# Kernel tuning notes

Hardware: AMD Instinct MI355X
Metric: run time of the kernel (lower is better)

The kernel has to match this reference:

```python
import jax, jax.numpy as jnp
import numpy as np
import math

D_MODEL = 1024
N_HEADS = 16
D_K = D_MODEL // N_HEADS
NB_FEATURES = max(1, math.ceil(math.log(D_MODEL)))  # 7
D_FF = 4096
BH = 4  # block_size_h
BW = 4  # block_size_w
EPS_LN = 1e-6


def gelu_approx(x):
    c = math.sqrt(2.0 / math.pi)
    return 0.5 * x * (1.0 + jnp.tanh(c * (x + 0.044715 * x * x * x)))


def layer_norm(x, alpha, bias):
    # torch .std() uses ddof=1 (unbiased)
    mean = x.mean(axis=-1, keepdims=True)
    std = jnp.std(x, axis=-1, ddof=1, keepdims=True)
    return alpha * (x - mean) / (std + EPS_LN) + bias


def causal_performer(q_in, k_in, v_in, wq, wk, wv, wo, omega):
    B, Sq, D = q_in.shape
    Sk = k_in.shape[1]
    q = (q_in @ wq.T).reshape(B, Sq, N_HEADS, D_K)
    k = (k_in @ wk.T).reshape(B, Sk, N_HEADS, D_K)
    v = (v_in @ wv.T).reshape(B, Sk, N_HEADS, D_K)
    # exp kernel feature map: exp(-0.5 * (x @ omega^T)^2)
    qp = jnp.exp(-0.5 * jnp.square(q @ omega.T))  # (B,Sq,H,nb)
    kp = jnp.exp(-0.5 * jnp.square(k @ omega.T))  # (B,Sk,H,nb)
    qp = qp / (qp.sum(-1, keepdims=True) + 1e-6)
    kp = kp / (kp.sum(-1, keepdims=True) + 1e-6)
    K_cum = jnp.cumsum(kp, axis=1)                               # (B,Sk,H,nb)
    KV_cum = jnp.cumsum(kp[..., None] * v[..., None, :], axis=1)  # (B,Sk,H,nb,dk)
    key_idx = jnp.clip((jnp.arange(Sq) // BH + 1) * BW - 1, None, Sk - 1)
    K_sel = K_cum[:, key_idx]    # (B,Sq,H,nb)
    KV_sel = KV_cum[:, key_idx]  # (B,Sq,H,nb,dk)
    num = jnp.einsum('bshn,bshnd->bshd', qp, KV_sel)
    den = jnp.einsum('bshn,bshn->bsh', qp, K_sel)[..., None]
    out = (num / (den + 1e-6)).reshape(B, Sq, D)
    return out @ wo.T


def setup_inputs() -> dict:
    key = jax.random.key(0)
    ks = jax.random.split(key, 24)
    s = 0.02
    p = {}
    p['x'] = jax.random.normal(ks[0], (2, 4096, D_MODEL), jnp.float32)
    p['lto'] = jax.random.normal(ks[1], (2, 4096, D_MODEL), jnp.float32)
    for i, nm in enumerate(['wq_s', 'wk_s', 'wv_s', 'wo_s']):
        p[nm] = jax.random.normal(ks[2 + i], (D_MODEL, D_MODEL), jnp.float32) * s
    for i, nm in enumerate(['wq_c', 'wk_c', 'wv_c', 'wo_c']):
        p[nm] = jax.random.normal(ks[6 + i], (D_MODEL, D_MODEL), jnp.float32) * s
    p['omega_s'] = jax.random.normal(ks[10], (NB_FEATURES, D_K), jnp.float32) / math.sqrt(D_K)
    p['omega_c'] = jax.random.normal(ks[11], (NB_FEATURES, D_K), jnp.float32) / math.sqrt(D_K)
    p['w1'] = jax.random.normal(ks[12], (D_FF, D_MODEL), jnp.float32) * s
    p['b1'] = jnp.zeros((D_FF,), jnp.float32)
    p['w2'] = jax.random.normal(ks[13], (D_MODEL, D_FF), jnp.float32) * s
    p['b2'] = jnp.zeros((D_MODEL,), jnp.float32)
    for i in range(3):
        p[f'ln{i}_a'] = jnp.ones((D_MODEL,), jnp.float32)
        p[f'ln{i}_b'] = jnp.zeros((D_MODEL,), jnp.float32)
    return p


def reference(x, lto, wq_s, wk_s, wv_s, wo_s, wq_c, wk_c, wv_c, wo_c,
              omega_s, omega_c, w1, b1, w2, b2,
              ln0_a, ln0_b, ln1_a, ln1_b, ln2_a, ln2_b):
    # residual 0: self-attention on x
    xn = layer_norm(x, ln0_a, ln0_b)
    x = x + causal_performer(xn, xn, xn, wq_s, wk_s, wv_s, wo_s, omega_s)
    # residual 1: cross-attention, queries = normed lto, keys/values = updated x
    ln = layer_norm(lto, ln1_a, ln1_b)
    lto = lto + causal_performer(ln, x, x, wq_c, wk_c, wv_c, wo_c, omega_c)
    # residual 2: feed-forward
    fn = layer_norm(lto, ln2_a, ln2_b)
    ff = gelu_approx(fn @ w1.T + b1) @ w2.T + b2
    return lto + ff
```

## Files before the change

### kernel.cpp

```cpp
#include <hip/hip_runtime.h>
#include <cstdint>
#include <cstddef>

typedef __bf16 bf16;
typedef __bf16 bf16x8 __attribute__((ext_vector_type(8)));
typedef __bf16 bf16x4 __attribute__((ext_vector_type(4)));
typedef float  f32x4  __attribute__((ext_vector_type(4)));

#define NB 7
static constexpr int Bq = 2, Sq = 4096, Dm = 1024, Dff = 4096;
static constexpr int Mrows = Bq * Sq;
static constexpr int NCH = Sq / 4;
static constexpr int CSW = 464;

template <int V> struct ic { static constexpr int value = V; };

__device__ __forceinline__ void gload16(const void* g, void* l) {
  __builtin_amdgcn_global_load_lds((__attribute__((address_space(1))) void*)g,
                                   (__attribute__((address_space(3))) void*)l,
                                   16, 0, 0);
}

template <int N> __device__ __forceinline__ void wait_vmcnt() {
  asm volatile("s_waitcnt vmcnt(%0)" :: "n"(N) : "memory");
}
__device__ __forceinline__ void wait_lgkm0() {
  asm volatile("s_waitcnt lgkmcnt(0)" ::: "memory");
}
__device__ __forceinline__ void SB() { __builtin_amdgcn_sched_barrier(0); }

__device__ __forceinline__ float gelu_f(float x) {
  const float c = 0.79788456080286535588f;
  float z = c * (x + 0.044715f * x * x * x);
  float t = 1.f - 2.f / (__expf(2.f * z) + 1.f);
  return 0.5f * x * (1.f + t);
}

struct CvtA {
  const float* s[10];
  bf16* d[10];
  int start[11];
};
__global__ __launch_bounds__(256) void cvt10(CvtA a) {
  const int i = blockIdx.x * 256 + threadIdx.x;
  int r = 0;
#pragma unroll
  for (int k = 1; k < 10; ++k) r += (i >= a.start[k]);
  const int o = i - a.start[r];
  f32x4 v = *(const f32x4*)&a.s[r][(size_t)o * 4];
  bf16x4 ov;
#pragma unroll
  for (int e = 0; e < 4; ++e) ov[e] = (bf16)v[e];
  *(bf16x4*)&a.d[r][(size_t)o * 4] = ov;
}

__global__ __launch_bounds__(256) void ln_kernel(const float* __restrict__ x,
                                                 const float* __restrict__ alpha,
                                                 const float* __restrict__ beta,
                                                 bf16* __restrict__ out) {
  const int row = blockIdx.x, tid = threadIdx.x;
  const float* xr = x + (size_t)row * Dm;
  f32x4 v = *(const f32x4*)&xr[tid * 4];
  float s  = v[0] + v[1] + v[2] + v[3];
  float s2 = v[0]*v[0] + v[1]*v[1] + v[2]*v[2] + v[3]*v[3];
#pragma unroll
  for (int o = 32; o > 0; o >>= 1) { s += __shfl_xor(s, o); s2 += __shfl_xor(s2, o); }
  __shared__ float red[8];
  const int wid = tid >> 6, lane = tid & 63;
  if (lane == 0) { red[wid] = s; red[wid + 4] = s2; }
  __syncthreads();
  s  = red[0] + red[1] + red[2] + red[3];
  s2 = red[4] + red[5] + red[6] + red[7];
  const float mean = s * (1.f / 1024.f);
  float var = (s2 - s * mean) * (1.f / 1023.f);
  var = fmaxf(var, 0.f);
  const float inv = 1.f / (sqrtf(var) + 1e-6f);
  f32x4 a4 = *(const f32x4*)&alpha[tid * 4];
  f32x4 b4 = *(const f32x4*)&beta[tid * 4];
  bf16x4 o4;
#pragma unroll
  for (int e = 0; e < 4; ++e) o4[e] = (bf16)(a4[e] * (v[e] - mean) * inv + b4[e]);
  *(bf16x4*)&out[(size_t)row * Dm + tid * 4] = o4;
}

template <int MODE>
__global__ __launch_bounds__(256, 2) void gemm128(
    const bf16* __restrict__ A, const bf16* __restrict__ Bw,
    int M, int N, int K,
    const float* __restrict__ bias, const float* __restrict__ res,
    float* __restrict__ outF, bf16* __restrict__ outB) {
  __shared__ __align__(16) char lds[65536];

  const int tid = threadIdx.x;
  const int lane = tid & 63, wid = tid >> 6;
  const int wm = wid >> 1, wn = wid & 1;

  const int nwg = gridDim.x;
  const int nc = N >> 7;
  const int nsc = nc >> 3;
  const int lin = (blockIdx.x & 7) * (nwg >> 3) + (blockIdx.x >> 3);
  const int s = lin >> 6, w = lin & 63;
  const int sr = s / nsc, sc = s - sr * nsc;
  const int bm = (sr * 8 + (w >> 3)) * 128;
  const int bn = (sc * 8 + (w & 7)) * 128;
  const int NT = K >> 6;

  const int srow = tid >> 3;
  const int scol = ((tid & 7) ^ (srow & 7)) * 8;
  const bf16* pSA = A  + (size_t)(bm + srow) * K + scol;
  const bf16* pSB = Bw + (size_t)(bn + srow) * K + scol;
  const size_t cK = (size_t)32 * K;
  const int stDa = wid * 1024;

  auto stage = [&](int buf, const bf16* sa, const bf16* sb) {
#pragma unroll
    for (int c = 0; c < 4; ++c) {
      gload16(sa + (size_t)c * cK, &lds[buf * 16384 + c * 4096 + stDa]);
      gload16(sb + (size_t)c * cK, &lds[32768 + buf * 16384 + c * 4096 + stDa]);
    }
  };

  const int lr = lane & 15, uo = lane >> 4;
  const int rdA0 = (wm * 64 + lr) * 128 + ((uo)     ^ (lr & 7)) * 16;
  const int rdA1 = (wm * 64 + lr) * 128 + ((4 + uo) ^ (lr & 7)) * 16;
  const int rdB0 = 32768 + (wn * 64 + lr) * 128 + ((uo)     ^ (lr & 7)) * 16;
  const int rdB1 = 32768 + (wn * 64 + lr) * 128 + ((4 + uo) ^ (lr & 7)) * 16;

  f32x4 acc[4][4] = {};
  bf16x8 a[4][2], b[4][2];

  stage(0, pSA, pSB);
  stage(1, pSA + 64, pSB + 64);
  pSA += 128; pSB += 128;
  wait_vmcnt<8>();
  __builtin_amdgcn_s_barrier();

  auto TILE = [&](auto BUFC, int tt) {
    constexpr int BUF = decltype(BUFC)::value;
#pragma unroll
    for (int i = 0; i < 4; ++i) {
      a[i][0] = *(const bf16x8*)&lds[rdA0 + BUF * 16384 + i * 2048];
      a[i][1] = *(const bf16x8*)&lds[rdA1 + BUF * 16384 + i * 2048];
    }
#pragma unroll
    for (int j = 0; j < 4; ++j) {
      b[j][0] = *(const bf16x8*)&lds[rdB0 + BUF * 16384 + j * 2048];
      b[j][1] = *(const bf16x8*)&lds[rdB1 + BUF * 16384 + j * 2048];
    }
    wait_lgkm0(); SB();
    __builtin_amdgcn_s_barrier(); SB();

    if (tt + 2 < NT) stage(BUF, pSA + (size_t)(tt & 1) * 64,
                                pSB + (size_t)(tt & 1) * 64);
#pragma unroll
    for (int i = 0; i < 4; ++i)
#pragma unroll
      for (int j = 0; j < 4; ++j) {
        acc[i][j] = __builtin_amdgcn_mfma_f32_16x16x32_bf16(a[i][0], b[j][0], acc[i][j], 0, 0, 0);
        acc[i][j] = __builtin_amdgcn_mfma_f32_16x16x32_bf16(a[i][1], b[j][1], acc[i][j], 0, 0, 0);
      }
    SB();
    if (tt < NT - 2) wait_vmcnt<8>();
    else             wait_vmcnt<0>();
    __builtin_amdgcn_s_barrier(); SB();
  };

  for (int t = 0; t < NT; t += 2) {
    TILE(ic<0>{}, t);
    TILE(ic<1>{}, t + 1);
    pSA += 128; pSB += 128;
  }

#pragma unroll
  for (int f = 0; f < 4; ++f) {
    const int r0 = bm + wm * 64 + f * 16 + (lane >> 4) * 4;
#pragma unroll
    for (int g = 0; g < 4; ++g) {
      const int c = bn + wn * 64 + g * 16 + (lane & 15);
      float bv = 0.f;
      if (MODE == 3 || MODE == 4) bv = bias[c];
#pragma unroll
      for (int r = 0; r < 4; ++r) {
        const size_t idx = (size_t)(r0 + r) * N + c;
        float v = acc[f][g][r];
        if (MODE == 1 || MODE == 2) v += res[idx];
        if (MODE == 3) v = gelu_f(v + bv);
        if (MODE == 4) v += bv + res[idx];
        if (MODE == 0 || MODE == 1 || MODE == 3) outB[idx] = (bf16)v;
        else outF[idx] = v;
      }
    }
  }
}

__global__ __launch_bounds__(512) void perf_cs(
    const bf16* __restrict__ kmat, const bf16* __restrict__ vmat, int ld,
    const float* __restrict__ omega, bf16* __restrict__ CS,
    float* __restrict__ segtot) {
  const int tid = threadIdx.x;
  const int bh = blockIdx.y, b = bh >> 4, h = bh & 15;
  const int seg = blockIdx.x;
  const int s0 = seg * 512;
  __shared__ __align__(16) bf16 vs[512][64];
  __shared__ float kps[512][8];
  __shared__ float oms[448];

  {
    const bf16* vb = vmat + ((size_t)(b * Sq + s0)) * ld + h * 64;
#pragma unroll
    for (int p = 0; p < 8; ++p) {
      const int row = p * 64 + (tid >> 3), c16 = (tid & 7) * 8;
      *(uint4*)&vs[row][c16 ^ ((row & 7) * 8)] =
          *(const uint4*)&vb[(size_t)row * ld + c16];
    }
  }
  if (tid < 448) oms[tid] = omega[tid];
  __syncthreads();

  {
    const int row = tid;
    const bf16* kr = kmat + ((size_t)(b * Sq + s0 + row)) * ld + h * 64;
    bf16x8 kv[8];
#pragma unroll
    for (int q = 0; q < 8; ++q) kv[q] = *(const bf16x8*)&kr[q * 8];
    float f[NB];
#pragma unroll
    for (int n = 0; n < NB; ++n) f[n] = 0.f;
#pragma unroll
    for (int d = 0; d < 64; ++d) {
      const float kd = (float)kv[d >> 3][d & 7];
#pragma unroll
      for (int n = 0; n < NB; ++n) f[n] += kd * oms[n * 64 + d];
    }
    float sum = 1e-6f, e[NB];
#pragma unroll
    for (int n = 0; n < NB; ++n) { e[n] = __expf(-0.5f * f[n] * f[n]); sum += e[n]; }
    const float inv = 1.f / sum;
#pragma unroll
    for (int n = 0; n < NB; ++n) kps[row][n] = e[n] * inv;
    kps[row][7] = 0.f;
  }
  __syncthreads();

  if (tid < CSW) {
    const int comp = tid;
    bf16* outb = CS + ((size_t)bh * NCH + seg * 128) * CSW;
    float r = 0.f;
    if (comp < 8) {
      for (int c = 0; c < 128; ++c) {
        if (comp < 7)
          r += kps[4*c][comp] + kps[4*c+1][comp] + kps[4*c+2][comp] + kps[4*c+3][comp];
        outb[(size_t)c * CSW + comp] = (bf16)r;
      }
    } else if (comp < 456) {
      const int n = (comp - 8) >> 6, d = (comp - 8) & 63;
      for (int c = 0; c < 128; ++c) {
#pragma unroll
        for (int i = 0; i < 4; ++i) {
          const int row = 4 * c + i;
          r += kps[row][n] * (float)vs[row][d ^ ((row & 7) * 8)];
        }
        outb[(size_t)c * CSW + comp] = (bf16)r;
      }
    } else {
      for (int c = 0; c < 128; ++c) outb[(size_t)c * CSW + comp] = (bf16)0.f;
    }
    segtot[((size_t)bh * 8 + seg) * CSW + comp] = r;
  }
}

__global__ __launch_bounds__(256) void perf_out(
    const bf16* __restrict__ qmat, int ldq, const float* __restrict__ omega,
    const bf16* __restrict__ CS, const float* __restrict__ segtot,
    bf16* __restrict__ attn) {
  const int tid = threadIdx.x;
  const int bh = blockIdx.y, b = bh >> 4, h = bh & 15;
  const int s0 = blockIdx.x * 128;
  const int cg0 = s0 >> 2;
  const int seg = cg0 >> 7;
  __shared__ __align__(16) float Ps[32 * CSW];
  __shared__ float qps[128][8];
  __shared__ float oms[NB * 64];
  __shared__ float offs[CSW];

  for (int c = tid; c < CSW; c += 256) {
    float o = 0.f;
    for (int ss = 0; ss < seg; ++ss) o += segtot[((size_t)bh * 8 + ss) * CSW + c];
    offs[c] = o;
  }
  if (tid < 224) { oms[tid] = omega[tid]; oms[tid + 224] = omega[tid + 224]; }
  __syncthreads();

  {
    const bf16* src = CS + ((size_t)bh * NCH + cg0) * CSW;
    for (int i = tid; i < 32 * CSW / 4; i += 256) {
      bf16x4 a4 = *(const bf16x4*)&src[(size_t)i * 4];
      const int c0 = (i % (CSW / 4)) * 4;
      f32x4 o;
#pragma unroll
      for (int e = 0; e < 4; ++e) o[e] = (float)a4[e] + offs[c0 + e];
      *(f32x4*)&Ps[i * 4] = o;
    }
  }
  __syncthreads();
  {
    const int p = tid >> 1, half = tid & 1;
    const bf16* qr = qmat + ((size_t)(b * Sq + s0 + p)) * ldq + h * 64 + half * 32;
    bf16x8 qv[4];
#pragma unroll
    for (int q = 0; q < 4; ++q) qv[q] = *(const bf16x8*)&qr[q * 8];
    float f[NB];
#pragma unroll
    for (int n = 0; n < NB; ++n) f[n] = 0.f;
#pragma unroll
    for (int d = 0; d < 32; ++d) {
      float qd = (float)qv[d >> 3][d & 7];
#pragma unroll
      for (int n = 0; n < NB; ++n) f[n] += qd * oms[n * 64 + half * 32 + d];
    }
    float sum = 1e-6f;
    float e[NB];
#pragma unroll
    for (int n = 0; n < NB; ++n) {
      float full = f[n] + __shfl_xor(f[n], 1);
      e[n] = __expf(-0.5f * full * full);
      sum += e[n];
    }
    float inv = 1.f / sum;
    if (half == 0) {
      float den = 1e-6f;
      const float* Pr = &Ps[(p >> 2) * CSW];
#pragma unroll
      for (int n = 0; n < NB; ++n) {
        float qn = e[n] * inv;
        qps[p][n] = qn;
        den += qn * Pr[n];
      }
      qps[p][7] = 1.f / den;
    }
  }
  __syncthreads();
  {
    const int d = tid & 63, w = tid >> 6;
    for (int qq = w; qq < 128; qq += 4) {
      const float* Pr = &Ps[(qq >> 2) * CSW + 8 + d];
      float num = 0.f;
#pragma unroll
      for (int n = 0; n < NB; ++n) num += qps[qq][n] * Pr[n * 64];
      attn[((size_t)(b * Sq + s0 + qq)) * Dm + h * 64 + d] = (bf16)(num * qps[qq][7]);
    }
  }
}

extern "C" void kernel_launch(void* const* d_in, const int* in_sizes, int n_in,
                              void* d_out, int out_size, void* d_ws, size_t ws_size,
                              hipStream_t stream) {
  const float* x    = (const float*)d_in[0];
  const float* lto  = (const float*)d_in[1];
  const float* w_s[4] = {(const float*)d_in[2], (const float*)d_in[3],
                         (const float*)d_in[4], (const float*)d_in[5]};
  const float* w_c[4] = {(const float*)d_in[6], (const float*)d_in[7],
                         (const float*)d_in[8], (const float*)d_in[9]};
  const float* omega_s = (const float*)d_in[10];
  const float* omega_c = (const float*)d_in[11];
  const float* w1 = (const float*)d_in[12];
  const float* b1 = (const float*)d_in[13];
  const float* w2 = (const float*)d_in[14];
  const float* b2 = (const float*)d_in[15];
  const float* ln_a[3] = {(const float*)d_in[16], (const float*)d_in[18], (const float*)d_in[20]};
  const float* ln_b[3] = {(const float*)d_in[17], (const float*)d_in[19], (const float*)d_in[21]};

  char* ws = (char*)d_ws;
  size_t off = 0;
  auto alloc = [&](size_t bytes) -> char* {
    char* p = ws + off;
    off += (bytes + 255) & ~(size_t)255;
    return p;
  };

  const size_t actB = (size_t)Mrows * Dm * sizeof(bf16);
  const size_t MB32 = (size_t)Mrows * 2048 * sizeof(bf16);

  bf16* wqkv = (bf16*)alloc((size_t)3072 * 1024 * 2);
  bf16* wo_sb = (bf16*)alloc((size_t)1024 * 1024 * 2);
  bf16* wq_cb = (bf16*)alloc((size_t)1024 * 1024 * 2);
  bf16* wkv  = (bf16*)alloc((size_t)2048 * 1024 * 2);
  bf16* wo_cb = (bf16*)alloc((size_t)1024 * 1024 * 2);
  bf16* w1b = (bf16*)alloc((size_t)Dff * Dm * 2);
  bf16* w2b = (bf16*)alloc((size_t)Dff * Dm * 2);
  bf16* xnb  = (bf16*)alloc(actB);
  char* pool = alloc((size_t)Mrows * Dff * 2);
  bf16* qkvb = (bf16*)pool;
  bf16* kvb  = (bf16*)pool;
  bf16* qb   = (bf16*)(pool + MB32);
  bf16* hb   = (bf16*)pool;
  bf16* attnb= (bf16*)alloc(actB);
  bf16* x2b  = (bf16*)alloc(actB);
  bf16* ln1b = (bf16*)alloc(actB);
  float* lto2 = (float*)alloc((size_t)Mrows * Dm * 4);
  bf16*  CSb  = (bf16*)alloc((size_t)32 * NCH * CSW * 2);
  float* stb  = (float*)alloc((size_t)32 * 8 * CSW * 4);
  bf16* fnb = xnb;

  {
    CvtA a;
    const float* srcs[10] = {w_s[0], w_s[1], w_s[2], w_s[3], w_c[0],
                             w_c[1], w_c[2], w_c[3], w1, w2};
    bf16* dsts[10] = {wqkv, wqkv + 1048576, wqkv + 2097152, wo_sb, wq_cb,
                      wkv, wkv + 1048576, wo_cb, w1b, w2b};
    const int SM = 262144, LG = 1048576;
    int st = 0;
    for (int i = 0; i < 10; ++i) {
      a.s[i] = srcs[i]; a.d[i] = dsts[i]; a.start[i] = st;
      st += (i < 8) ? SM : LG;
    }
    a.start[10] = st;
    cvt10<<<st / 256, 256, 0, stream>>>(a);
  }

  dim3 gperf(Sq / 128, Bq * 16);
  dim3 gseg(8, Bq * 16);
  const int gQKV = (Mrows / 128) * (3072 / 128);
  const int gKV  = (Mrows / 128) * (2048 / 128);
  const int gFF1 = (Mrows / 128) * (4096 / 128);
  const int gN1k = (Mrows / 128) * (1024 / 128);

  ln_kernel<<<Mrows, 256, 0, stream>>>(x, ln_a[0], ln_b[0], xnb);
  gemm128<0><<<gQKV, 256, 0, stream>>>(xnb, wqkv, Mrows, 3072, 1024, nullptr, nullptr, nullptr, qkvb);
  perf_cs<<<gseg, 512, 0, stream>>>(qkvb + 1024, qkvb + 2048, 3072, omega_s, CSb, stb);
  perf_out<<<gperf, 256, 0, stream>>>(qkvb, 3072, omega_s, CSb, stb, attnb);
  gemm128<1><<<gN1k, 256, 0, stream>>>(attnb, wo_sb, Mrows, 1024, 1024, nullptr, x, nullptr, x2b);

  ln_kernel<<<Mrows, 256, 0, stream>>>(lto, ln_a[1], ln_b[1], ln1b);
  gemm128<0><<<gN1k, 256, 0, stream>>>(ln1b, wq_cb, Mrows, 1024, 1024, nullptr, nullptr, nullptr, qb);
  gemm128<0><<<gKV, 256, 0, stream>>>(x2b, wkv, Mrows, 2048, 1024, nullptr, nullptr, nullptr, kvb);
  perf_cs<<<gseg, 512, 0, stream>>>(kvb, kvb + 1024, 2048, omega_c, CSb, stb);
  perf_out<<<gperf, 256, 0, stream>>>(qb, 1024, omega_c, CSb, stb, attnb);
  gemm128<2><<<gN1k, 256, 0, stream>>>(attnb, wo_cb, Mrows, 1024, 1024, nullptr, lto, lto2, nullptr);

  ln_kernel<<<Mrows, 256, 0, stream>>>(lto2, ln_a[2], ln_b[2], fnb);
  gemm128<3><<<gFF1, 256, 0, stream>>>(fnb, w1b, Mrows, 4096, 1024, b1, nullptr, nullptr, hb);
  gemm128<4><<<gN1k, 256, 0, stream>>>(hb, w2b, Mrows, 1024, 4096, b2, lto2, (float*)d_out, nullptr);
}
```

Measured before the change: 500.0 us.

## Add 256x256-tile GEMM kernel for wide QKV, KV and FF1 projections

Adds a 512-thread GEMM with 256x256 output tiles, 128 KB of double-buffered LDS and an 8x4 MFMA fragment per wave. It is used for the QKV, KV and FF1 GEMMs, with the GELU-plus-bias epilogue moved there from the 128-tile kernel. Larger tiles raise arithmetic intensity per LDS and global load and cut the number of workgroups. In exchange, only one block fits per CU, register pressure rises, and the QKV grid of 384 tiles leaves a partial second wave.

Measured after the change: 529.0 us. 5.8% more time.

```diff
diff --git a/kernel.cpp b/kernel.cpp
--- a/kernel.cpp
+++ b/kernel.cpp
@@ -84,6 +84,112 @@
 }
 
 template <int MODE>
+__global__ __launch_bounds__(512, 2) void gemm256(
+    const bf16* __restrict__ A, const bf16* __restrict__ Bw,
+    int M, int N, int K,
+    const float* __restrict__ bias, bf16* __restrict__ outB) {
+  __shared__ __align__(16) char lds[131072];
+
+  const int tid = threadIdx.x;
+  const int lane = tid & 63, wid = tid >> 6;
+  const int wm = wid >> 2, wn = wid & 3;
+
+  const int nwg = gridDim.x;
+  const int nc = N >> 8;
+  const int nsc = nc >> 2;
+  const int lin = (blockIdx.x & 7) * (nwg >> 3) + (blockIdx.x >> 3);
+  const int s = lin >> 4, w = lin & 15;
+  const int sr = s / nsc, sc = s - sr * nsc;
+  const int bm = (sr * 4 + (w >> 2)) * 256;
+  const int bn = (sc * 4 + (w & 3)) * 256;
+  const int NT = K >> 6;
+
+  const int srow = tid >> 3;
+  const int scol = ((tid & 7) ^ (srow & 7)) * 8;
+  const bf16* pSA = A  + (size_t)(bm + srow) * K + scol;
+  const bf16* pSB = Bw + (size_t)(bn + srow) * K + scol;
+  const size_t cK = (size_t)64 * K;
+  const int stDa = wid * 1024;
+
+  auto stage = [&](int buf, const bf16* sa, const bf16* sb) {
+#pragma unroll
+    for (int c = 0; c < 4; ++c) {
+      gload16(sa + (size_t)c * cK, &lds[buf * 32768 + c * 8192 + stDa]);
+      gload16(sb + (size_t)c * cK, &lds[65536 + buf * 32768 + c * 8192 + stDa]);
+    }
+  };
+
+  const int lr = lane & 15, uo = lane >> 4;
+  const int rA0 = (wm * 128 + lr) * 128 + ((uo)     ^ (lr & 7)) * 16;
+  const int rA1 = (wm * 128 + lr) * 128 + ((4 + uo) ^ (lr & 7)) * 16;
+  const int rB0 = 65536 + (wn * 64 + lr) * 128 + ((uo)     ^ (lr & 7)) * 16;
+  const int rB1 = 65536 + (wn * 64 + lr) * 128 + ((4 + uo) ^ (lr & 7)) * 16;
+
+  f32x4 acc[8][4] = {};
+  bf16x8 a[8][2], b[4][2];
+
+  stage(0, pSA, pSB);
+  stage(1, pSA + 64, pSB + 64);
+  pSA += 128; pSB += 128;
+  wait_vmcnt<8>();
+  __builtin_amdgcn_s_barrier();
+
+  auto TILE = [&](auto BUFC, int tt) {
+    constexpr int BUF = decltype(BUFC)::value;
+#pragma unroll
+    for (int i = 0; i < 8; ++i) {
+      a[i][0] = *(const bf16x8*)&lds[rA0 + BUF * 32768 + i * 2048];
+      a[i][1] = *(const bf16x8*)&lds[rA1 + BUF * 32768 + i * 2048];
+    }
+#pragma unroll
+    for (int j = 0; j < 4; ++j) {
+      b[j][0] = *(const bf16x8*)&lds[rB0 + BUF * 32768 + j * 2048];
+      b[j][1] = *(const bf16x8*)&lds[rB1 + BUF * 32768 + j * 2048];
+    }
+    wait_lgkm0(); SB();
+    __builtin_amdgcn_s_barrier(); SB();
+
+    if (tt + 2 < NT) stage(BUF, pSA + (size_t)(tt & 1) * 64,
+                                pSB + (size_t)(tt & 1) * 64);
+#pragma unroll
+    for (int i = 0; i < 8; ++i)
+#pragma unroll
+      for (int j = 0; j < 4; ++j) {
+        acc[i][j] = __builtin_amdgcn_mfma_f32_16x16x32_bf16(a[i][0], b[j][0], acc[i][j], 0, 0, 0);
+        acc[i][j] = __builtin_amdgcn_mfma_f32_16x16x32_bf16(a[i][1], b[j][1], acc[i][j], 0, 0, 0);
+      }
+    SB();
+    if (tt < NT - 2) wait_vmcnt<8>();
+    else             wait_vmcnt<0>();
+    __builtin_amdgcn_s_barrier(); SB();
+  };
+
+  for (int t = 0; t < NT; t += 2) {
+    TILE(ic<0>{}, t);
+    TILE(ic<1>{}, t + 1);
+    pSA += 128; pSB += 128;
+  }
+
+#pragma unroll
+  for (int f = 0; f < 8; ++f) {
+    const int r0 = bm + wm * 128 + f * 16 + (lane >> 4) * 4;
+#pragma unroll
+    for (int g = 0; g < 4; ++g) {
+      const int c = bn + wn * 64 + g * 16 + (lane & 15);
+      float bv = 0.f;
+      if (MODE == 3) bv = bias[c];
+#pragma unroll
+      for (int r = 0; r < 4; ++r) {
+        const size_t idx = (size_t)(r0 + r) * N + c;
+        float v = acc[f][g][r];
+        if (MODE == 3) v = gelu_f(v + bv);
+        outB[idx] = (bf16)v;
+      }
+    }
+  }
+}
+
+template <int MODE>
 __global__ __launch_bounds__(256, 2) void gemm128(
     const bf16* __restrict__ A, const bf16* __restrict__ Bw,
     int M, int N, int K,
@@ -178,15 +284,14 @@
     for (int g = 0; g < 4; ++g) {
       const int c = bn + wn * 64 + g * 16 + (lane & 15);
       float bv = 0.f;
-      if (MODE == 3 || MODE == 4) bv = bias[c];
+      if (MODE == 4) bv = bias[c];
 #pragma unroll
       for (int r = 0; r < 4; ++r) {
         const size_t idx = (size_t)(r0 + r) * N + c;
         float v = acc[f][g][r];
         if (MODE == 1 || MODE == 2) v += res[idx];
-        if (MODE == 3) v = gelu_f(v + bv);
         if (MODE == 4) v += bv + res[idx];
-        if (MODE == 0 || MODE == 1 || MODE == 3) outB[idx] = (bf16)v;
+        if (MODE == 0 || MODE == 1) outB[idx] = (bf16)v;
         else outF[idx] = v;
       }
     }
@@ -420,25 +525,25 @@
 
   dim3 gperf(Sq / 128, Bq * 16);
   dim3 gseg(8, Bq * 16);
-  const int gQKV = (Mrows / 128) * (3072 / 128);
-  const int gKV  = (Mrows / 128) * (2048 / 128);
-  const int gFF1 = (Mrows / 128) * (4096 / 128);
+  const int gQKV = (Mrows / 256) * (3072 / 256);
+  const int gKV  = (Mrows / 256) * (2048 / 256);
+  const int gFF1 = (Mrows / 256) * (4096 / 256);
   const int gN1k = (Mrows / 128) * (1024 / 128);
 
   ln_kernel<<<Mrows, 256, 0, stream>>>(x, ln_a[0], ln_b[0], xnb);
-  gemm128<0><<<gQKV, 256, 0, stream>>>(xnb, wqkv, Mrows, 3072, 1024, nullptr, nullptr, nullptr, qkvb);
+  gemm256<0><<<gQKV, 512, 0, stream>>>(xnb, wqkv, Mrows, 3072, 1024, nullptr, qkvb);
   perf_cs<<<gseg, 512, 0, stream>>>(qkvb + 1024, qkvb + 2048, 3072, omega_s, CSb, stb);
   perf_out<<<gperf, 256, 0, stream>>>(qkvb, 3072, omega_s, CSb, stb, attnb);
   gemm128<1><<<gN1k, 256, 0, stream>>>(attnb, wo_sb, Mrows, 1024, 1024, nullptr, x, nullptr, x2b);
 
   ln_kernel<<<Mrows, 256, 0, stream>>>(lto, ln_a[1], ln_b[1], ln1b);
   gemm128<0><<<gN1k, 256, 0, stream>>>(ln1b, wq_cb, Mrows, 1024, 1024, nullptr, nullptr, nullptr, qb);
-  gemm128<0><<<gKV, 256, 0, stream>>>(x2b, wkv, Mrows, 2048, 1024, nullptr, nullptr, nullptr, kvb);
+  gemm256<0><<<gKV, 512, 0, stream>>>(x2b, wkv, Mrows, 2048, 1024, nullptr, kvb);
   perf_cs<<<gseg, 512, 0, stream>>>(kvb, kvb + 1024, 2048, omega_c, CSb, stb);
   perf_out<<<gperf, 256, 0, stream>>>(qb, 1024, omega_c, CSb, stb, attnb);
   gemm128<2><<<gN1k, 256, 0, stream>>>(attnb, wo_cb, Mrows, 1024, 1024, nullptr, lto, lto2, nullptr);
 
   ln_kernel<<<Mrows, 256, 0, stream>>>(lto2, ln_a[2], ln_b[2], fnb);
-  gemm128<3><<<gFF1, 256, 0, stream>>>(fnb, w1b, Mrows, 4096, 1024, b1, nullptr, nullptr, hb);
+  gemm256<3><<<gFF1, 512, 0, stream>>>(fnb, w1b, Mrows, 4096, 1024, b1, hb);
   gemm128<4><<<gN1k, 256, 0, stream>>>(hb, w2b, Mrows, 1024, 4096, b2, lto2, (float*)d_out, nullptr);
 }
```

## Replace double-buffered GEMM pipeline with single-buffered loop and higher occupancy

Applied to the files above, without the earlier changes.

The bf16 GEMM drops its two-stage LDS double buffer, with its explicit vmcnt waits and sched barriers, and uses a simple loop. Each K-tile is loaded into a single 32 KB LDS buffer between two __syncthreads, then consumed by the MFMAs. Halving LDS and raising launch_bounds to 3 blocks per CU is meant to rely on more resident workgroups to hide memory latency. The cost is that each workgroup no longer overlaps its own global loads with compute, and it now takes two full barriers per tile.

Measured after the change: 532.7 us. 6.5% more time.

```diff
diff --git a/kernel.cpp b/kernel.cpp
--- a/kernel.cpp
+++ b/kernel.cpp
@@ -13,21 +13,11 @@
 static constexpr int NCH = Sq / 4;
 static constexpr int CSW = 464;
 
-template <int V> struct ic { static constexpr int value = V; };
-
 __device__ __forceinline__ void gload16(const void* g, void* l) {
   __builtin_amdgcn_global_load_lds((__attribute__((address_space(1))) void*)g,
                                    (__attribute__((address_space(3))) void*)l,
                                    16, 0, 0);
 }
-
-template <int N> __device__ __forceinline__ void wait_vmcnt() {
-  asm volatile("s_waitcnt vmcnt(%0)" :: "n"(N) : "memory");
-}
-__device__ __forceinline__ void wait_lgkm0() {
-  asm volatile("s_waitcnt lgkmcnt(0)" ::: "memory");
-}
-__device__ __forceinline__ void SB() { __builtin_amdgcn_sched_barrier(0); }
 
 __device__ __forceinline__ float gelu_f(float x) {
   const float c = 0.79788456080286535588f;
@@ -84,12 +74,12 @@
 }
 
 template <int MODE>
-__global__ __launch_bounds__(256, 2) void gemm128(
+__global__ __launch_bounds__(256, 3) void gemm128(
     const bf16* __restrict__ A, const bf16* __restrict__ Bw,
     int M, int N, int K,
     const float* __restrict__ bias, const float* __restrict__ res,
     float* __restrict__ outF, bf16* __restrict__ outB) {
-  __shared__ __align__(16) char lds[65536];
+  __shared__ __align__(16) char lds[32768];
 
   const int tid = threadIdx.x;
   const int lane = tid & 63, wid = tid >> 6;
@@ -112,46 +102,34 @@
   const size_t cK = (size_t)32 * K;
   const int stDa = wid * 1024;
 
-  auto stage = [&](int buf, const bf16* sa, const bf16* sb) {
-#pragma unroll
-    for (int c = 0; c < 4; ++c) {
-      gload16(sa + (size_t)c * cK, &lds[buf * 16384 + c * 4096 + stDa]);
-      gload16(sb + (size_t)c * cK, &lds[32768 + buf * 16384 + c * 4096 + stDa]);
-    }
-  };
-
   const int lr = lane & 15, uo = lane >> 4;
   const int rdA0 = (wm * 64 + lr) * 128 + ((uo)     ^ (lr & 7)) * 16;
   const int rdA1 = (wm * 64 + lr) * 128 + ((4 + uo) ^ (lr & 7)) * 16;
-  const int rdB0 = 32768 + (wn * 64 + lr) * 128 + ((uo)     ^ (lr & 7)) * 16;
-  const int rdB1 = 32768 + (wn * 64 + lr) * 128 + ((4 + uo) ^ (lr & 7)) * 16;
+  const int rdB0 = 16384 + (wn * 64 + lr) * 128 + ((uo)     ^ (lr & 7)) * 16;
+  const int rdB1 = 16384 + (wn * 64 + lr) * 128 + ((4 + uo) ^ (lr & 7)) * 16;
 
   f32x4 acc[4][4] = {};
-  bf16x8 a[4][2], b[4][2];
-
-  stage(0, pSA, pSB);
-  stage(1, pSA + 64, pSB + 64);
-  pSA += 128; pSB += 128;
-  wait_vmcnt<8>();
-  __builtin_amdgcn_s_barrier();
-
-  auto TILE = [&](auto BUFC, int tt) {
-    constexpr int BUF = decltype(BUFC)::value;
+
+  for (int t = 0; t < NT; ++t) {
+    __syncthreads();
+#pragma unroll
+    for (int c = 0; c < 4; ++c) {
+      gload16(pSA + (size_t)c * cK, &lds[c * 4096 + stDa]);
+      gload16(pSB + (size_t)c * cK, &lds[16384 + c * 4096 + stDa]);
+    }
+    __syncthreads();
+
+    bf16x8 a[4][2], b[4][2];
 #pragma unroll
     for (int i = 0; i < 4; ++i) {
-      a[i][0] = *(const bf16x8*)&lds[rdA0 + BUF * 16384 + i * 2048];
-      a[i][1] = *(const bf16x8*)&lds[rdA1 + BUF * 16384 + i * 2048];
+      a[i][0] = *(const bf16x8*)&lds[rdA0 + i * 2048];
+      a[i][1] = *(const bf16x8*)&lds[rdA1 + i * 2048];
     }
 #pragma unroll
     for (int j = 0; j < 4; ++j) {
-      b[j][0] = *(const bf16x8*)&lds[rdB0 + BUF * 16384 + j * 2048];
-      b[j][1] = *(const bf16x8*)&lds[rdB1 + BUF * 16384 + j * 2048];
-    }
-    wait_lgkm0(); SB();
-    __builtin_amdgcn_s_barrier(); SB();
-
-    if (tt + 2 < NT) stage(BUF, pSA + (size_t)(tt & 1) * 64,
-                                pSB + (size_t)(tt & 1) * 64);
+      b[j][0] = *(const bf16x8*)&lds[rdB0 + j * 2048];
+      b[j][1] = *(const bf16x8*)&lds[rdB1 + j * 2048];
+    }
 #pragma unroll
     for (int i = 0; i < 4; ++i)
 #pragma unroll
@@ -159,16 +137,7 @@
         acc[i][j] = __builtin_amdgcn_mfma_f32_16x16x32_bf16(a[i][0], b[j][0], acc[i][j], 0, 0, 0);
         acc[i][j] = __builtin_amdgcn_mfma_f32_16x16x32_bf16(a[i][1], b[j][1], acc[i][j], 0, 0, 0);
       }
-    SB();
-    if (tt < NT - 2) wait_vmcnt<8>();
-    else             wait_vmcnt<0>();
-    __builtin_amdgcn_s_barrier(); SB();
-  };
-
-  for (int t = 0; t < NT; t += 2) {
-    TILE(ic<0>{}, t);
-    TILE(ic<1>{}, t + 1);
-    pSA += 128; pSB += 128;
+    pSA += 64; pSB += 64;
   }
 
 #pragma unroll
```

## Widen GEMM tiles to 128x256 with 32-wide K steps

Applied to the files above, without the earlier changes.

Replaces the 128x128x64 GEMM tile with a 128x256 tile using a 32-element K step. Each wave computes a 64x128 sub-tile, which raises MFMA work per LDS load of A and halves the number of workgroups. The change trades higher register use and more barriers per K for better operand reuse, and risks under-filling the GPU on the N=1024 GEMMs.

Measured after the change: 538.3 us. 1.08x slower.

```diff
diff --git a/kernel.cpp b/kernel.cpp
--- a/kernel.cpp
+++ b/kernel.cpp
@@ -84,83 +84,75 @@
 }
 
 template <int MODE>
-__global__ __launch_bounds__(256, 2) void gemm128(
+__global__ __launch_bounds__(256, 2) void gemmW(
     const bf16* __restrict__ A, const bf16* __restrict__ Bw,
     int M, int N, int K,
     const float* __restrict__ bias, const float* __restrict__ res,
     float* __restrict__ outF, bf16* __restrict__ outB) {
-  __shared__ __align__(16) char lds[65536];
+  __shared__ __align__(16) char lds[49152];
 
   const int tid = threadIdx.x;
   const int lane = tid & 63, wid = tid >> 6;
   const int wm = wid >> 1, wn = wid & 1;
 
   const int nwg = gridDim.x;
-  const int nc = N >> 7;
-  const int nsc = nc >> 3;
+  const int nc = N >> 8;
+  const int nsc = nc >> 2;
   const int lin = (blockIdx.x & 7) * (nwg >> 3) + (blockIdx.x >> 3);
   const int s = lin >> 6, w = lin & 63;
   const int sr = s / nsc, sc = s - sr * nsc;
-  const int bm = (sr * 8 + (w >> 3)) * 128;
-  const int bn = (sc * 8 + (w & 7)) * 128;
-  const int NT = K >> 6;
-
-  const int srow = tid >> 3;
-  const int scol = ((tid & 7) ^ (srow & 7)) * 8;
-  const bf16* pSA = A  + (size_t)(bm + srow) * K + scol;
-  const bf16* pSB = Bw + (size_t)(bn + srow) * K + scol;
-  const size_t cK = (size_t)32 * K;
-  const int stDa = wid * 1024;
-
-  auto stage = [&](int buf, const bf16* sa, const bf16* sb) {
-#pragma unroll
-    for (int c = 0; c < 4; ++c) {
-      gload16(sa + (size_t)c * cK, &lds[buf * 16384 + c * 4096 + stDa]);
-      gload16(sb + (size_t)c * cK, &lds[32768 + buf * 16384 + c * 4096 + stDa]);
-    }
+  const int bm = (sr * 16 + (w >> 2)) * 128;
+  const int bn = (sc * 4 + (w & 3)) * 256;
+  const int NT = K >> 5;
+
+  const int srow4 = tid >> 2;
+  const int cu = ((tid & 3) ^ ((srow4 >> 1) & 3)) * 8;
+  const bf16* pSA = A  + (size_t)(bm + srow4) * K + cu;
+  const bf16* pSB = Bw + (size_t)(bn + srow4) * K + cu;
+  const size_t swK = (size_t)64 * K;
+  const int dA = wid * 1024 + (lane & 63) * 16;
+
+  auto stage = [&](int buf, int t) {
+#pragma unroll
+    for (int s2 = 0; s2 < 2; ++s2)
+      gload16(pSA + s2 * swK + (size_t)t * 32, &lds[buf * 8192 + s2 * 4096 + dA]);
+#pragma unroll
+    for (int s2 = 0; s2 < 4; ++s2)
+      gload16(pSB + s2 * swK + (size_t)t * 32, &lds[16384 + buf * 16384 + s2 * 4096 + dA]);
   };
 
   const int lr = lane & 15, uo = lane >> 4;
-  const int rdA0 = (wm * 64 + lr) * 128 + ((uo)     ^ (lr & 7)) * 16;
-  const int rdA1 = (wm * 64 + lr) * 128 + ((4 + uo) ^ (lr & 7)) * 16;
-  const int rdB0 = 32768 + (wn * 64 + lr) * 128 + ((uo)     ^ (lr & 7)) * 16;
-  const int rdB1 = 32768 + (wn * 64 + lr) * 128 + ((4 + uo) ^ (lr & 7)) * 16;
-
-  f32x4 acc[4][4] = {};
-  bf16x8 a[4][2], b[4][2];
-
-  stage(0, pSA, pSB);
-  stage(1, pSA + 64, pSB + 64);
-  pSA += 128; pSB += 128;
-  wait_vmcnt<8>();
+  const int swz = (lr >> 1) & 3;
+  const int rdA = (wm * 64 + lr) * 64 + ((uo ^ swz) * 16);
+  const int rdB = 16384 + (wn * 128 + lr) * 64 + ((uo ^ swz) * 16);
+
+  f32x4 acc[4][8] = {};
+  bf16x8 a[4], b[8];
+
+  stage(0, 0);
+  stage(1, 1);
+  wait_vmcnt<6>();
   __builtin_amdgcn_s_barrier();
 
   auto TILE = [&](auto BUFC, int tt) {
     constexpr int BUF = decltype(BUFC)::value;
 #pragma unroll
-    for (int i = 0; i < 4; ++i) {
-      a[i][0] = *(const bf16x8*)&lds[rdA0 + BUF * 16384 + i * 2048];
-      a[i][1] = *(const bf16x8*)&lds[rdA1 + BUF * 16384 + i * 2048];
-    }
-#pragma unroll
-    for (int j = 0; j < 4; ++j) {
-      b[j][0] = *(const bf16x8*)&lds[rdB0 + BUF * 16384 + j * 2048];
-      b[j][1] = *(const bf16x8*)&lds[rdB1 + BUF * 16384 + j * 2048];
-    }
+    for (int i = 0; i < 4; ++i)
+      a[i] = *(const bf16x8*)&lds[rdA + BUF * 8192 + i * 1024];
+#pragma unroll
+    for (int j = 0; j < 8; ++j)
+      b[j] = *(const bf16x8*)&lds[rdB + BUF * 16384 + j * 1024];
     wait_lgkm0(); SB();
     __builtin_amdgcn_s_barrier(); SB();
 
-    if (tt + 2 < NT) stage(BUF, pSA + (size_t)(tt & 1) * 64,
-                                pSB + (size_t)(tt & 1) * 64);
+    if (tt + 2 < NT) stage(BUF, tt + 2);
 #pragma unroll
     for (int i = 0; i < 4; ++i)
 #pragma unroll
-      for (int j = 0; j < 4; ++j) {
-        acc[i][j] = __builtin_amdgcn_mfma_f32_16x16x32_bf16(a[i][0], b[j][0], acc[i][j], 0, 0, 0);
-        acc[i][j] = __builtin_amdgcn_mfma_f32_16x16x32_bf16(a[i][1], b[j][1], acc[i][j], 0, 0, 0);
-      }
+      for (int j = 0; j < 8; ++j)
+        acc[i][j] = __builtin_amdgcn_mfma_f32_16x16x32_bf16(a[i], b[j], acc[i][j], 0, 0, 0);
     SB();
-    if (tt < NT - 2) wait_vmcnt<8>();
+    if (tt < NT - 2) wait_vmcnt<6>();
     else             wait_vmcnt<0>();
     __builtin_amdgcn_s_barrier(); SB();
   };
@@ -168,15 +160,14 @@
   for (int t = 0; t < NT; t += 2) {
     TILE(ic<0>{}, t);
     TILE(ic<1>{}, t + 1);
-    pSA += 128; pSB += 128;
   }
 
 #pragma unroll
   for (int f = 0; f < 4; ++f) {
     const int r0 = bm + wm * 64 + f * 16 + (lane >> 4) * 4;
 #pragma unroll
-    for (int g = 0; g < 4; ++g) {
-      const int c = bn + wn * 64 + g * 16 + (lane & 15);
+    for (int g = 0; g < 8; ++g) {
+      const int c = bn + wn * 128 + g * 16 + (lane & 15);
       float bv = 0.f;
       if (MODE == 3 || MODE == 4) bv = bias[c];
 #pragma unroll
@@ -420,25 +411,25 @@
 
   dim3 gperf(Sq / 128, Bq * 16);
   dim3 gseg(8, Bq * 16);
-  const int gQKV = (Mrows / 128) * (3072 / 128);
-  const int gKV  = (Mrows / 128) * (2048 / 128);
-  const int gFF1 = (Mrows / 128) * (4096 / 128);
-  const int gN1k = (Mrows / 128) * (1024 / 128);
+  const int gQKV = (Mrows / 128) * (3072 / 256);
+  const int gKV  = (Mrows / 128) * (2048 / 256);
+  const int gFF1 = (Mrows / 128) * (4096 / 256);
+  const int gN1k = (Mrows / 128) * (1024 / 256);
 
   ln_kernel<<<Mrows, 256, 0, stream>>>(x, ln_a[0], ln_b[0], xnb);
-  gemm128<0><<<gQKV, 256, 0, stream>>>(xnb, wqkv, Mrows, 3072, 1024, nullptr, nullptr, nullptr, qkvb);
+  gemmW<0><<<gQKV, 256, 0, stream>>>(xnb, wqkv, Mrows, 3072, 1024, nullptr, nullptr, nullptr, qkvb);
   perf_cs<<<gseg, 512, 0, stream>>>(qkvb + 1024, qkvb + 2048, 3072, omega_s, CSb, stb);
   perf_out<<<gperf, 256, 0, stream>>>(qkvb, 3072, omega_s, CSb, stb, attnb);
-  gemm128<1><<<gN1k, 256, 0, stream>>>(attnb, wo_sb, Mrows, 1024, 1024, nullptr, x, nullptr, x2b);
+  gemmW<1><<<gN1k, 256, 0, stream>>>(attnb, wo_sb, Mrows, 1024, 1024, nullptr, x, nullptr, x2b);
 
   ln_kernel<<<Mrows, 256, 0, stream>>>(lto, ln_a[1], ln_b[1], ln1b);
-  gemm128<0><<<gN1k, 256, 0, stream>>>(ln1b, wq_cb, Mrows, 1024, 1024, nullptr, nullptr, nullptr, qb);
-  gemm128<0><<<gKV, 256, 0, stream>>>(x2b, wkv, Mrows, 2048, 1024, nullptr, nullptr, nullptr, kvb);
+  gemmW<0><<<gN1k, 256, 0, stream>>>(ln1b, wq_cb, Mrows, 1024, 1024, nullptr, nullptr, nullptr, qb);
+  gemmW<0><<<gKV, 256, 0, stream>>>(x2b, wkv, Mrows, 2048, 1024, nullptr, nullptr, nullptr, kvb);
   perf_cs<<<gseg, 512, 0, stream>>>(kvb, kvb + 1024, 2048, omega_c, CSb, stb);
   perf_out<<<gperf, 256, 0, stream>>>(qb, 1024, omega_c, CSb, stb, attnb);
-  gemm128<2><<<gN1k, 256, 0, stream>>>(attnb, wo_cb, Mrows, 1024, 1024, nullptr, lto, lto2, nullptr);
+  gemmW<2><<<gN1k, 256, 0, stream>>>(attnb, wo_cb, Mrows, 1024, 1024, nullptr, lto, lto2, nullptr);
 
   ln_kernel<<<Mrows, 256, 0, stream>>>(lto2, ln_a[2], ln_b[2], fnb);
-  gemm128<3><<<gFF1, 256, 0, stream>>>(fnb, w1b, Mrows, 4096, 1024, b1, nullptr, nullptr, hb);
-  gemm128<4><<<gN1k, 256, 0, stream>>>(hb, w2b, Mrows, 1024, 4096, b2, lto2, (float*)d_out, nullptr);
-}
+  gemmW<3><<<gFF1, 256, 0, stream>>>(fnb, w1b, Mrows, 4096, 1024, b1, nullptr, nullptr, hb);
+  gemmW<4><<<gN1k, 256, 0, stream>>>(hb, w2b, Mrows, 1024, 4096, b2, lto2, (float*)d_out, nullptr);
+}
```
